# Performance work log

Measured on AMD Instinct MI355X. Metric: run time of the kernel, lower is better.

The kernel has to match this reference:

```python
import jax, jax.numpy as jnp
import numpy as np

N = 30000      # num nodes
E = 600000     # num edges
D = 128        # feature dim (all layers)
R = 7          # num_relation
G = 16         # num graphs in batch
L = 3          # num layers (hidden_dims = [128,128,128])


def setup_inputs() -> dict:
    key = jax.random.key(0)
    ks = jax.random.split(key, 10)
    x = jax.random.normal(ks[0], (N, D), dtype=jnp.float32)
    node_in = jax.random.randint(ks[1], (E,), 0, N)
    node_out = jax.random.randint(ks[2], (E,), 0, N)
    relation = jax.random.randint(ks[3], (E,), 0, R)
    edge_weight = jax.random.uniform(ks[4], (E,), dtype=jnp.float32)
    node2graph = jnp.sort(jax.random.randint(ks[5], (N,), 0, G))
    # learned params: per-layer relational linear (R*D -> D) and self-loop linear (D -> D)
    Wr = jax.random.normal(ks[6], (L, R * D, D), dtype=jnp.float32) * 0.02
    br = jnp.zeros((L, D), dtype=jnp.float32)
    Wl = jax.random.normal(ks[7], (L, D, D), dtype=jnp.float32) * 0.02
    bl = jnp.zeros((L, D), dtype=jnp.float32)
    return dict(x=x, node_in=node_in, node_out=node_out, relation=relation,
                edge_weight=edge_weight, node2graph=node2graph,
                Wr=Wr, br=br, Wl=Wl, bl=bl)


def reference(x, node_in, node_out, relation, edge_weight, node2graph, Wr, br, Wl, bl):
    # relation-indexed destination segment: node_out * R + relation
    seg = node_out * R + relation            # (E,)
    ew = edge_weight[:, None]                # (E, 1)
    h = x
    for i in range(L):
        msg = h[node_in] * ew                                         # gather + weight, (E, D)
        upd = jax.ops.segment_sum(msg, seg, num_segments=N * R)       # scatter_add, (N*R, D)
        upd = upd.reshape(N, R * D)                                   # per-relation concat
        h = jax.nn.relu(upd @ Wr[i] + br[i] + h @ Wl[i] + bl[i])      # linear + self-loop + act
    node_feature = h                                                  # (N, D)
    graph_feature = jax.ops.segment_sum(node_feature, node2graph, num_segments=G)  # sum readout
    return graph_feature, node_feature
```

## Files before the change

### kernel.cpp

```cpp
#include <hip/hip_runtime.h>
#include <hip/hip_bf16.h>

#define NN 30000
#define NE 600000
#define DD 128
#define RR 7
#define GG 16
#define LL 3

#define NB64 ((NN + 63) / 64)

typedef short bf16x8 __attribute__((ext_vector_type(8)));
typedef float f32x4  __attribute__((ext_vector_type(4)));

__device__ __forceinline__ unsigned short f2bf(float f) {
    unsigned u = __float_as_uint(f);
    unsigned r = (u + 0x7fffu + ((u >> 16) & 1u)) >> 16;
    return (unsigned short)r;
}
__device__ __forceinline__ float bf2f(unsigned short b) {
    return __uint_as_float(((unsigned)b) << 16);
}
__device__ __forceinline__ ushort2 pk2bf(float a, float b) {
    __hip_bfloat162 t = __float22bfloat162_rn(make_float2(a, b));
    return *(ushort2*)&t;
}

__device__ __forceinline__ void gl_lds16(const void* g, void* l) {
    __builtin_amdgcn_global_load_lds(
        (const __attribute__((address_space(1))) void*)g,
        (__attribute__((address_space(3))) void*)l, 16, 0, 0);
}

__global__ __launch_bounds__(256) void pack_weights(
    const float* __restrict__ Wl,
    const float* __restrict__ Wr,
    unsigned short* __restrict__ Bw)
{
    int t = blockIdx.x * 256 + threadIdx.x;
    if (t >= LL * 1024 * DD) return;
    int l = t >> 17;
    int rem = t & 131071;
    int n = rem >> 7;
    int k = rem & 127;
    float v;
    if (n < DD) {
        v = Wl[(size_t)l * DD * DD + k * DD + n];
    } else {
        int q = n - DD;
        v = Wr[(size_t)l * RR * DD * DD + (size_t)((q >> 7) * DD + k) * DD + (q & 127)];
    }
    Bw[(size_t)l * 1024 * DD + n * DD + k] = f2bf(v);
}

__global__ __launch_bounds__(256) void convert_bf16(
    const float* __restrict__ in, unsigned short* __restrict__ out, int n4)
{
    int i = blockIdx.x * 256 + threadIdx.x;
    if (i >= n4) return;
    float4 v = ((const float4*)in)[i];
    ushort2 lo = pk2bf(v.x, v.y);
    ushort2 hi = pk2bf(v.z, v.w);
    ((ushort4*)out)[i] = make_ushort4(lo.x, lo.y, hi.x, hi.y);
}

#define ASTR 128
__global__ __launch_bounds__(256) void gemm_mfma(
    const unsigned short* __restrict__ hb,
    const unsigned short* __restrict__ Bw,
    const float* __restrict__ br,
    const float* __restrict__ bl,
    unsigned short* __restrict__ haccb,
    unsigned short* __restrict__ Zb,
    int N)
{
    __shared__ unsigned short As[64 * ASTR];
    __shared__ unsigned short Bs[128 * ASTR];

    const int tid  = threadIdx.x;
    const int wave = tid >> 6;
    const int lane = tid & 63;
    const int quad = lane >> 4;
    const int l16  = lane & 15;
    const int row0 = blockIdx.x * 64;
    const int col0 = blockIdx.y * 128;

#pragma unroll
    for (int i = 0; i < 4; ++i) {
        int g = i * 4 + wave;
        gl_lds16(hb + (size_t)(row0 + g * 4) * DD + lane * 8,
                 As + g * 512);
    }
#pragma unroll
    for (int i = 0; i < 8; ++i) {
        int g = i * 4 + wave;
        gl_lds16(Bw + (size_t)col0 * DD + (size_t)g * 512 + lane * 8,
                 Bs + g * 512);
    }
    __syncthreads();

    f32x4 acc[4][2];
#pragma unroll
    for (int mt = 0; mt < 4; ++mt)
#pragma unroll
        for (int nt = 0; nt < 2; ++nt)
            acc[mt][nt] = (f32x4){0.f, 0.f, 0.f, 0.f};

    const unsigned short* As_l = As + l16 * ASTR;
    const unsigned short* Bs_l = Bs + (wave * 32 + l16) * ASTR;

#pragma unroll
    for (int kc = 0; kc < 4; ++kc) {
        int ko = kc * 32 + quad * 8;
        bf16x8 a0 = *(const bf16x8*)(As_l + 0 * 16 * ASTR + ko);
        bf16x8 a1 = *(const bf16x8*)(As_l + 1 * 16 * ASTR + ko);
        bf16x8 a2 = *(const bf16x8*)(As_l + 2 * 16 * ASTR + ko);
        bf16x8 a3 = *(const bf16x8*)(As_l + 3 * 16 * ASTR + ko);
        bf16x8 b0 = *(const bf16x8*)(Bs_l + 0 * 16 * ASTR + ko);
        bf16x8 b1 = *(const bf16x8*)(Bs_l + 1 * 16 * ASTR + ko);
        acc[0][0] = __builtin_amdgcn_mfma_f32_16x16x32_bf16(a0, b0, acc[0][0], 0, 0, 0);
        acc[1][0] = __builtin_amdgcn_mfma_f32_16x16x32_bf16(a1, b0, acc[1][0], 0, 0, 0);
        acc[2][0] = __builtin_amdgcn_mfma_f32_16x16x32_bf16(a2, b0, acc[2][0], 0, 0, 0);
        acc[3][0] = __builtin_amdgcn_mfma_f32_16x16x32_bf16(a3, b0, acc[3][0], 0, 0, 0);
        acc[0][1] = __builtin_amdgcn_mfma_f32_16x16x32_bf16(a0, b1, acc[0][1], 0, 0, 0);
        acc[1][1] = __builtin_amdgcn_mfma_f32_16x16x32_bf16(a1, b1, acc[1][1], 0, 0, 0);
        acc[2][1] = __builtin_amdgcn_mfma_f32_16x16x32_bf16(a2, b1, acc[2][1], 0, 0, 0);
        acc[3][1] = __builtin_amdgcn_mfma_f32_16x16x32_bf16(a3, b1, acc[3][1], 0, 0, 0);
    }

    const int ncol = wave * 32 + l16;
    if (col0 == 0) {
        float bias0 = br[ncol] + bl[ncol];
        float bias1 = br[ncol + 16] + bl[ncol + 16];
#pragma unroll
        for (int mt = 0; mt < 4; ++mt) {
#pragma unroll
            for (int reg = 0; reg < 4; ++reg) {
                int row = row0 + mt * 16 + quad * 4 + reg;
                if (row < N) {
                    ushort2 p = pk2bf(acc[mt][0][reg] + bias0,
                                      acc[mt][1][reg] + bias1);
                    haccb[(size_t)row * DD + ncol]      = p.x;
                    haccb[(size_t)row * DD + ncol + 16] = p.y;
                }
            }
        }
    } else {
        const int zc = col0 - DD + ncol;
#pragma unroll
        for (int mt = 0; mt < 4; ++mt) {
#pragma unroll
            for (int reg = 0; reg < 4; ++reg) {
                int row = row0 + mt * 16 + quad * 4 + reg;
                if (row < N) {
                    ushort2 p = pk2bf(acc[mt][0][reg], acc[mt][1][reg]);
                    Zb[(size_t)row * (RR * DD) + zc]      = p.x;
                    Zb[(size_t)row * (RR * DD) + zc + 16] = p.y;
                }
            }
        }
    }
}

__global__ __launch_bounds__(256) void bucket_hist(
    const int* __restrict__ node_out, int* __restrict__ bcnt, int E)
{
    int e = blockIdx.x * 256 + threadIdx.x;
    if (e < E) atomicAdd(&bcnt[(node_out[e] >> 6) * 16], 1);
}

__global__ __launch_bounds__(512) void bucket_scan(
    const int* __restrict__ bcnt, int* __restrict__ bstart,
    int* __restrict__ bcur, int nb)
{
    __shared__ int s[512];
    int t = threadIdx.x;
    int v = (t < nb) ? bcnt[t * 16] : 0;
    s[t] = v;
    __syncthreads();
#pragma unroll
    for (int off = 1; off < 512; off <<= 1) {
        int u = (t >= off) ? s[t - off] : 0;
        __syncthreads();
        s[t] += u;
        __syncthreads();
    }
    if (t <= nb) {
        int excl = s[t] - v;
        bstart[t] = excl;
        if (t < nb) bcur[t * 16] = excl;
    }
}

__global__ __launch_bounds__(256) void bucket_scatter(
    const int* __restrict__ node_in,
    const int* __restrict__ node_out,
    const int* __restrict__ relation,
    const float* __restrict__ ew,
    int* __restrict__ bcur,
    int2* __restrict__ tmp,
    int E)
{
    int e = blockIdx.x * 256 + threadIdx.x;
    if (e >= E) return;
    int o = node_out[e];
    int pos = atomicAdd(&bcur[(o >> 6) * 16], 1);
    tmp[pos] = make_int2(((o & 63) << 18) | (node_in[e] << 3) | relation[e],
                         __float_as_int(ew[e]));
}

__global__ __launch_bounds__(256) void bucket_sort(
    const int2* __restrict__ tmp,
    const int* __restrict__ bstart,
    int2* __restrict__ meta,
    int* __restrict__ start,
    int N)
{
    __shared__ int hist[64];
    __shared__ int scan[64];
    __shared__ int cur[64];
    const int b = blockIdx.x;
    const int t = threadIdx.x;
    const int s0 = bstart[b];
    const int s1 = bstart[b + 1];

    if (t < 64) hist[t] = 0;
    __syncthreads();
    for (int i = s0 + t; i < s1; i += 256)
        atomicAdd(&hist[((unsigned)tmp[i].x) >> 18], 1);
    __syncthreads();

    int v = (t < 64) ? hist[t] : 0;
    if (t < 64) scan[t] = v;
    __syncthreads();
#pragma unroll
    for (int off = 1; off < 64; off <<= 1) {
        int u = (t < 64 && t >= off) ? scan[t - off] : 0;
        __syncthreads();
        if (t < 64) scan[t] += u;
        __syncthreads();
    }
    if (t < 64) {
        int excl = scan[t] - v;
        cur[t] = s0 + excl;
        int node = b * 64 + t;
        if (node <= N) start[node] = s0 + excl;
    }
    __syncthreads();

    for (int i = s0 + t; i < s1; i += 256) {
        int2 m = tmp[i];
        int j = ((unsigned)m.x) >> 18;
        int pos = atomicAdd(&cur[j], 1);
        int key = m.x & 0x3ffff;
        int in = key >> 3, rel = key & 7;
        meta[pos] = make_int2((in * RR + rel) << 7, m.y);
    }
}

__global__ __launch_bounds__(256) void aggregate(
    const unsigned short* __restrict__ Zb,
    const int* __restrict__ start,
    const int2* __restrict__ meta,
    const unsigned short* __restrict__ haccb,
    float* __restrict__ out_f32,
    unsigned short* __restrict__ out_bf16,
    int N)
{
    int wid = (blockIdx.x * 256 + threadIdx.x) >> 6;
    int lane = threadIdx.x & 63;
    if (wid >= N) return;

    int e0 = start[wid];
    int e1 = start[wid + 1];

    float accx = 0.f, accy = 0.f;
    int e = e0;
    for (; e + 8 <= e1; e += 8) {
        unsigned u[8]; float wt[8];
#pragma unroll
        for (int j = 0; j < 8; ++j) {
            int2 m = meta[e + j];
            u[j] = *(const unsigned*)(Zb + m.x + lane * 2);
            wt[j] = __int_as_float(m.y);
        }
#pragma unroll
        for (int j = 0; j < 8; ++j) {
            accx = fmaf(wt[j], __uint_as_float(u[j] << 16), accx);
            accy = fmaf(wt[j], __uint_as_float(u[j] & 0xffff0000u), accy);
        }
    }
    for (; e + 2 <= e1; e += 2) {
        int2 m0 = meta[e];
        int2 m1 = meta[e + 1];
        unsigned u0 = *(const unsigned*)(Zb + m0.x + lane * 2);
        unsigned u1 = *(const unsigned*)(Zb + m1.x + lane * 2);
        float w0 = __int_as_float(m0.y), w1 = __int_as_float(m1.y);
        accx = fmaf(w0, __uint_as_float(u0 << 16), accx);
        accy = fmaf(w0, __uint_as_float(u0 & 0xffff0000u), accy);
        accx = fmaf(w1, __uint_as_float(u1 << 16), accx);
        accy = fmaf(w1, __uint_as_float(u1 & 0xffff0000u), accy);
    }
    if (e < e1) {
        int2 m = meta[e];
        unsigned u = *(const unsigned*)(Zb + m.x + lane * 2);
        float wt = __int_as_float(m.y);
        accx = fmaf(wt, __uint_as_float(u << 16), accx);
        accy = fmaf(wt, __uint_as_float(u & 0xffff0000u), accy);
    }

    unsigned bu = *(const unsigned*)(haccb + (size_t)wid * DD + lane * 2);
    float ox = fmaxf(bf2f((unsigned short)(bu & 0xffffu)) + accx, 0.f);
    float oy = fmaxf(bf2f((unsigned short)(bu >> 16)) + accy, 0.f);
    if (out_f32) {
        *(float2*)(out_f32 + (size_t)wid * DD + lane * 2) = make_float2(ox, oy);
    }
    if (out_bf16) {
        ushort2 o = pk2bf(ox, oy);
        *(ushort2*)(out_bf16 + (size_t)wid * DD + lane * 2) = o;
    }
}

__global__ __launch_bounds__(256) void graph_sum(
    const float* __restrict__ nf,
    const int* __restrict__ n2g,
    float* __restrict__ gf,
    int N)
{
    int t = blockIdx.x * 256 + threadIdx.x;
    int chunk = t >> 5;
    int lane = t & 31;
    int n0 = chunk * 16;
    if (n0 >= N) return;
    int nend = n0 + 16; if (nend > N) nend = N;

    float4 acc = make_float4(0.f, 0.f, 0.f, 0.f);
    int curg = n2g[n0];
    for (int n = n0; n < nend; ++n) {
        int g = n2g[n];
        if (g != curg) {
            float* dst = gf + (size_t)curg * DD + lane * 4;
            atomicAdd(dst + 0, acc.x); atomicAdd(dst + 1, acc.y);
            atomicAdd(dst + 2, acc.z); atomicAdd(dst + 3, acc.w);
            acc = make_float4(0.f, 0.f, 0.f, 0.f);
            curg = g;
        }
        float4 v = *(const float4*)(nf + (size_t)n * DD + lane * 4);
        acc.x += v.x; acc.y += v.y; acc.z += v.z; acc.w += v.w;
    }
    float* dst = gf + (size_t)curg * DD + lane * 4;
    atomicAdd(dst + 0, acc.x); atomicAdd(dst + 1, acc.y);
    atomicAdd(dst + 2, acc.z); atomicAdd(dst + 3, acc.w);
}

extern "C" void kernel_launch(void* const* d_in, const int* in_sizes, int n_in,
                              void* d_out, int out_size, void* d_ws, size_t ws_size,
                              hipStream_t stream)
{
    const float* x        = (const float*)d_in[0];
    const int*   node_in  = (const int*)d_in[1];
    const int*   node_out = (const int*)d_in[2];
    const int*   relation = (const int*)d_in[3];
    const float* ew       = (const float*)d_in[4];
    const int*   n2g      = (const int*)d_in[5];
    const float* Wr       = (const float*)d_in[6];
    const float* br       = (const float*)d_in[7];
    const float* Wl       = (const float*)d_in[8];
    const float* bl       = (const float*)d_in[9];

    float* out = (float*)d_out;
    float* gf = out;
    float* nf = out + GG * DD;

    char* w = (char*)d_ws;
    unsigned short* Zb   = (unsigned short*)w; w += (size_t)NN * RR * DD * 2;
    unsigned short* haccb= (unsigned short*)w; w += (size_t)NN * DD * 2;
    unsigned short* hbA  = (unsigned short*)w; w += (size_t)NN * DD * 2;
    unsigned short* hbB  = (unsigned short*)w; w += (size_t)NN * DD * 2;
    unsigned short* Bw   = (unsigned short*)w; w += (size_t)LL * 1024 * DD * 2;
    int2*  meta   = (int2*)w;                  w += (size_t)NE * 8;
    int2*  tmp    = (int2*)w;                  w += (size_t)NE * 8;
    int*   start  = (int*)w;                   w += (size_t)(NN + 1) * 4 + 60;
    int*   bcnt   = (int*)w;                   w += (size_t)NB64 * 16 * 4 + 64;
    int*   bcur   = (int*)w;                   w += (size_t)NB64 * 16 * 4 + 64;
    int*   bstart = (int*)w;                   w += (size_t)(NB64 + 1) * 4 + 60;

    const int N = NN, E = NE;

    pack_weights<<<(LL * 1024 * DD + 255) / 256, 256, 0, stream>>>(Wl, Wr, Bw);
    convert_bf16<<<(N * DD / 4 + 255) / 256, 256, 0, stream>>>(x, hbA, N * DD / 4);

    hipMemsetAsync(bcnt, 0, (size_t)NB64 * 16 * sizeof(int), stream);
    bucket_hist<<<(E + 255) / 256, 256, 0, stream>>>(node_out, bcnt, E);
    bucket_scan<<<1, 512, 0, stream>>>(bcnt, bstart, bcur, NB64);
    bucket_scatter<<<(E + 255) / 256, 256, 0, stream>>>(
        node_in, node_out, relation, ew, bcur, tmp, E);
    bucket_sort<<<NB64, 256, 0, stream>>>(tmp, bstart, meta, start, N);

    dim3 ggrid((N + 63) / 64, 8);
    unsigned short* hin = hbA;
    unsigned short* hnext = hbB;
    for (int l = 0; l < LL; ++l) {
        const float* br_l = br + (size_t)l * DD;
        const float* bl_l = bl + (size_t)l * DD;
        const unsigned short* Bw_l = Bw + (size_t)l * 1024 * DD;

        gemm_mfma<<<ggrid, 256, 0, stream>>>(hin, Bw_l, br_l, bl_l, haccb, Zb, N);

        bool last = (l == LL - 1);
        aggregate<<<(N * 64 + 255) / 256, 256, 0, stream>>>(
            Zb, start, meta, haccb,
            last ? nf : (float*)nullptr,
            last ? (unsigned short*)nullptr : hnext, N);

        unsigned short* t = hin; hin = hnext; hnext = t;
    }

    hipMemsetAsync(gf, 0, (size_t)GG * DD * sizeof(float), stream);
    int chunks = (N + 15) / 16;
    graph_sum<<<(chunks * 32 + 255) / 256, 256, 0, stream>>>(nf, n2g, gf, N);
}
```

Measured before the change: 344.4 us.

## Aggregate raw features per relation before transforming with one fused GEMM

Swaps the order of the two steps. Each layer used to run the per-relation linear transform first and then gather the wide transformed rows for every edge. Now each node first gathers and sums the narrow bf16 input rows per (node, relation) into a message buffer, and a single GEMM with K=1024 then applies the relational and self-loop weights together, with bias and ReLU fused in. Per-edge gathers now hit a small feature table instead of the large transformed one. The bucket sort now orders edges by node and relation with per-relation start offsets, and the memsets are folded into existing kernels. The trade-offs are that the GEMM grid becomes 469 blocks doing an unpipelined K loop, and each wave's gather loop is split into seven short per-relation chains.

```diff
diff --git a/kernel.cpp b/kernel.cpp
--- a/kernel.cpp
+++ b/kernel.cpp
@@ -9,6 +9,8 @@
 #define LL 3
 
 #define NB64 ((NN + 63) / 64)
+#define NROW (NB64 * 64)
+#define MS   (RR * DD)
 
 typedef short bf16x8 __attribute__((ext_vector_type(8)));
 typedef float f32x4  __attribute__((ext_vector_type(4)));
@@ -18,9 +20,6 @@
     unsigned r = (u + 0x7fffu + ((u >> 16) & 1u)) >> 16;
     return (unsigned short)r;
 }
-__device__ __forceinline__ float bf2f(unsigned short b) {
-    return __uint_as_float(((unsigned)b) << 16);
-}
 __device__ __forceinline__ ushort2 pk2bf(float a, float b) {
     __hip_bfloat162 t = __float22bfloat162_rn(make_float2(a, b));
     return *(ushort2*)&t;
@@ -35,131 +34,37 @@
 __global__ __launch_bounds__(256) void pack_weights(
     const float* __restrict__ Wl,
     const float* __restrict__ Wr,
-    unsigned short* __restrict__ Bw)
+    unsigned short* __restrict__ Bw2,
+    int* __restrict__ bcnt)
 {
     int t = blockIdx.x * 256 + threadIdx.x;
-    if (t >= LL * 1024 * DD) return;
-    int l = t >> 17;
-    int rem = t & 131071;
-    int n = rem >> 7;
-    int k = rem & 127;
+    if (t < NB64 * 16) bcnt[t] = 0;
+    if (t >= LL * 8 * DD * DD) return;
+    int kp = t & 127;
+    int n  = (t >> 7) & 127;
+    int kc = (t >> 14) & 7;
+    int l  = t >> 17;
+    int k  = kc * 128 + kp;
     float v;
-    if (n < DD) {
-        v = Wl[(size_t)l * DD * DD + k * DD + n];
-    } else {
-        int q = n - DD;
-        v = Wr[(size_t)l * RR * DD * DD + (size_t)((q >> 7) * DD + k) * DD + (q & 127)];
-    }
-    Bw[(size_t)l * 1024 * DD + n * DD + k] = f2bf(v);
+    if (k < MS) v = Wr[(size_t)l * MS * DD + (size_t)k * DD + n];
+    else        v = Wl[(size_t)l * DD * DD + (size_t)(k - MS) * DD + n];
+    Bw2[(size_t)l * 8 * DD * DD + (size_t)kc * DD * DD + n * DD + kp] = f2bf(v);
 }
 
 __global__ __launch_bounds__(256) void convert_bf16(
-    const float* __restrict__ in, unsigned short* __restrict__ out, int n4)
+    const float* __restrict__ in, unsigned short* __restrict__ out,
+    float* __restrict__ gf, int n4)
 {
     int i = blockIdx.x * 256 + threadIdx.x;
+    if (blockIdx.x == 0) {
+#pragma unroll
+        for (int j = 0; j < 8; ++j) gf[threadIdx.x + j * 256] = 0.f;
+    }
     if (i >= n4) return;
     float4 v = ((const float4*)in)[i];
     ushort2 lo = pk2bf(v.x, v.y);
     ushort2 hi = pk2bf(v.z, v.w);
     ((ushort4*)out)[i] = make_ushort4(lo.x, lo.y, hi.x, hi.y);
-}
-
-#define ASTR 128
-__global__ __launch_bounds__(256) void gemm_mfma(
-    const unsigned short* __restrict__ hb,
-    const unsigned short* __restrict__ Bw,
-    const float* __restrict__ br,
-    const float* __restrict__ bl,
-    unsigned short* __restrict__ haccb,
-    unsigned short* __restrict__ Zb,
-    int N)
-{
-    __shared__ unsigned short As[64 * ASTR];
-    __shared__ unsigned short Bs[128 * ASTR];
-
-    const int tid  = threadIdx.x;
-    const int wave = tid >> 6;
-    const int lane = tid & 63;
-    const int quad = lane >> 4;
-    const int l16  = lane & 15;
-    const int row0 = blockIdx.x * 64;
-    const int col0 = blockIdx.y * 128;
-
-#pragma unroll
-    for (int i = 0; i < 4; ++i) {
-        int g = i * 4 + wave;
-        gl_lds16(hb + (size_t)(row0 + g * 4) * DD + lane * 8,
-                 As + g * 512);
-    }
-#pragma unroll
-    for (int i = 0; i < 8; ++i) {
-        int g = i * 4 + wave;
-        gl_lds16(Bw + (size_t)col0 * DD + (size_t)g * 512 + lane * 8,
-                 Bs + g * 512);
-    }
-    __syncthreads();
-
-    f32x4 acc[4][2];
-#pragma unroll
-    for (int mt = 0; mt < 4; ++mt)
-#pragma unroll
-        for (int nt = 0; nt < 2; ++nt)
-            acc[mt][nt] = (f32x4){0.f, 0.f, 0.f, 0.f};
-
-    const unsigned short* As_l = As + l16 * ASTR;
-    const unsigned short* Bs_l = Bs + (wave * 32 + l16) * ASTR;
-
-#pragma unroll
-    for (int kc = 0; kc < 4; ++kc) {
-        int ko = kc * 32 + quad * 8;
-        bf16x8 a0 = *(const bf16x8*)(As_l + 0 * 16 * ASTR + ko);
-        bf16x8 a1 = *(const bf16x8*)(As_l + 1 * 16 * ASTR + ko);
-        bf16x8 a2 = *(const bf16x8*)(As_l + 2 * 16 * ASTR + ko);
-        bf16x8 a3 = *(const bf16x8*)(As_l + 3 * 16 * ASTR + ko);
-        bf16x8 b0 = *(const bf16x8*)(Bs_l + 0 * 16 * ASTR + ko);
-        bf16x8 b1 = *(const bf16x8*)(Bs_l + 1 * 16 * ASTR + ko);
-        acc[0][0] = __builtin_amdgcn_mfma_f32_16x16x32_bf16(a0, b0, acc[0][0], 0, 0, 0);
-        acc[1][0] = __builtin_amdgcn_mfma_f32_16x16x32_bf16(a1, b0, acc[1][0], 0, 0, 0);
-        acc[2][0] = __builtin_amdgcn_mfma_f32_16x16x32_bf16(a2, b0, acc[2][0], 0, 0, 0);
-        acc[3][0] = __builtin_amdgcn_mfma_f32_16x16x32_bf16(a3, b0, acc[3][0], 0, 0, 0);
-        acc[0][1] = __builtin_amdgcn_mfma_f32_16x16x32_bf16(a0, b1, acc[0][1], 0, 0, 0);
-        acc[1][1] = __builtin_amdgcn_mfma_f32_16x16x32_bf16(a1, b1, acc[1][1], 0, 0, 0);
-        acc[2][1] = __builtin_amdgcn_mfma_f32_16x16x32_bf16(a2, b1, acc[2][1], 0, 0, 0);
-        acc[3][1] = __builtin_amdgcn_mfma_f32_16x16x32_bf16(a3, b1, acc[3][1], 0, 0, 0);
-    }
-
-    const int ncol = wave * 32 + l16;
-    if (col0 == 0) {
-        float bias0 = br[ncol] + bl[ncol];
-        float bias1 = br[ncol + 16] + bl[ncol + 16];
-#pragma unroll
-        for (int mt = 0; mt < 4; ++mt) {
-#pragma unroll
-            for (int reg = 0; reg < 4; ++reg) {
-                int row = row0 + mt * 16 + quad * 4 + reg;
-                if (row < N) {
-                    ushort2 p = pk2bf(acc[mt][0][reg] + bias0,
-                                      acc[mt][1][reg] + bias1);
-                    haccb[(size_t)row * DD + ncol]      = p.x;
-                    haccb[(size_t)row * DD + ncol + 16] = p.y;
-                }
-            }
-        }
-    } else {
-        const int zc = col0 - DD + ncol;
-#pragma unroll
-        for (int mt = 0; mt < 4; ++mt) {
-#pragma unroll
-            for (int reg = 0; reg < 4; ++reg) {
-                int row = row0 + mt * 16 + quad * 4 + reg;
-                if (row < N) {
-                    ushort2 p = pk2bf(acc[mt][0][reg], acc[mt][1][reg]);
-                    Zb[(size_t)row * (RR * DD) + zc]      = p.x;
-                    Zb[(size_t)row * (RR * DD) + zc + 16] = p.y;
-                }
-            }
-        }
-    }
 }
 
 __global__ __launch_bounds__(256) void bucket_hist(
@@ -205,7 +110,7 @@
     if (e >= E) return;
     int o = node_out[e];
     int pos = atomicAdd(&bcur[(o >> 6) * 16], 1);
-    tmp[pos] = make_int2(((o & 63) << 18) | (node_in[e] << 3) | relation[e],
+    tmp[pos] = make_int2(((o & 63) << 21) | (relation[e] << 18) | node_in[e],
                          __float_as_int(ew[e]));
 }
 
@@ -213,111 +118,205 @@
     const int2* __restrict__ tmp,
     const int* __restrict__ bstart,
     int2* __restrict__ meta,
-    int* __restrict__ start,
+    int* __restrict__ start2,
     int N)
 {
-    __shared__ int hist[64];
-    __shared__ int scan[64];
-    __shared__ int cur[64];
+    __shared__ int hist[512];
+    __shared__ int excl[512];
+    __shared__ int cur[512];
+    __shared__ int ssum[256];
     const int b = blockIdx.x;
     const int t = threadIdx.x;
     const int s0 = bstart[b];
     const int s1 = bstart[b + 1];
 
-    if (t < 64) hist[t] = 0;
+    hist[t] = 0; hist[t + 256] = 0;
     __syncthreads();
     for (int i = s0 + t; i < s1; i += 256)
         atomicAdd(&hist[((unsigned)tmp[i].x) >> 18], 1);
     __syncthreads();
 
-    int v = (t < 64) ? hist[t] : 0;
-    if (t < 64) scan[t] = v;
-    __syncthreads();
-#pragma unroll
-    for (int off = 1; off < 64; off <<= 1) {
-        int u = (t < 64 && t >= off) ? scan[t - off] : 0;
-        __syncthreads();
-        if (t < 64) scan[t] += u;
-        __syncthreads();
-    }
-    if (t < 64) {
-        int excl = scan[t] - v;
-        cur[t] = s0 + excl;
-        int node = b * 64 + t;
-        if (node <= N) start[node] = s0 + excl;
+    int a0 = hist[2 * t], a1 = hist[2 * t + 1];
+    ssum[t] = a0 + a1;
+    __syncthreads();
+#pragma unroll
+    for (int off = 1; off < 256; off <<= 1) {
+        int u = (t >= off) ? ssum[t - off] : 0;
+        __syncthreads();
+        ssum[t] += u;
+        __syncthreads();
+    }
+    int base = (t == 0) ? 0 : ssum[t - 1];
+    excl[2 * t] = base;
+    excl[2 * t + 1] = base + a0;
+    cur[2 * t] = s0 + base;
+    cur[2 * t + 1] = s0 + base + a0;
+    __syncthreads();
+
+    {
+        int node0 = b * 64 + (t >> 3) * 2;
+        int k0 = 2 * t, k1 = 2 * t + 1;
+        int n0 = b * 64 + (k0 >> 3), n1 = b * 64 + (k1 >> 3);
+        if (n0 < N) start2[n0 * 8 + (k0 & 7)] = s0 + excl[k0];
+        if (n1 < N) start2[n1 * 8 + (k1 & 7)] = s0 + excl[k1];
+        (void)node0;
     }
     __syncthreads();
 
     for (int i = s0 + t; i < s1; i += 256) {
         int2 m = tmp[i];
-        int j = ((unsigned)m.x) >> 18;
-        int pos = atomicAdd(&cur[j], 1);
-        int key = m.x & 0x3ffff;
-        int in = key >> 3, rel = key & 7;
-        meta[pos] = make_int2((in * RR + rel) << 7, m.y);
-    }
-}
-
-__global__ __launch_bounds__(256) void aggregate(
-    const unsigned short* __restrict__ Zb,
-    const int* __restrict__ start,
+        int key = ((unsigned)m.x) >> 18;
+        int pos = atomicAdd(&cur[key], 1);
+        int src = m.x & 0x3ffff;
+        meta[pos] = make_int2(src << 7, m.y);
+    }
+}
+
+__global__ __launch_bounds__(256) void aggregate_msg(
+    const unsigned short* __restrict__ hb,
+    const int* __restrict__ start2,
     const int2* __restrict__ meta,
-    const unsigned short* __restrict__ haccb,
-    float* __restrict__ out_f32,
-    unsigned short* __restrict__ out_bf16,
+    unsigned short* __restrict__ msg,
     int N)
 {
     int wid = (blockIdx.x * 256 + threadIdx.x) >> 6;
     int lane = threadIdx.x & 63;
     if (wid >= N) return;
 
-    int e0 = start[wid];
-    int e1 = start[wid + 1];
-
-    float accx = 0.f, accy = 0.f;
-    int e = e0;
-    for (; e + 8 <= e1; e += 8) {
-        unsigned u[8]; float wt[8];
-#pragma unroll
-        for (int j = 0; j < 8; ++j) {
-            int2 m = meta[e + j];
-            u[j] = *(const unsigned*)(Zb + m.x + lane * 2);
-            wt[j] = __int_as_float(m.y);
-        }
-#pragma unroll
-        for (int j = 0; j < 8; ++j) {
-            accx = fmaf(wt[j], __uint_as_float(u[j] << 16), accx);
-            accy = fmaf(wt[j], __uint_as_float(u[j] & 0xffff0000u), accy);
-        }
-    }
-    for (; e + 2 <= e1; e += 2) {
-        int2 m0 = meta[e];
-        int2 m1 = meta[e + 1];
-        unsigned u0 = *(const unsigned*)(Zb + m0.x + lane * 2);
-        unsigned u1 = *(const unsigned*)(Zb + m1.x + lane * 2);
-        float w0 = __int_as_float(m0.y), w1 = __int_as_float(m1.y);
-        accx = fmaf(w0, __uint_as_float(u0 << 16), accx);
-        accy = fmaf(w0, __uint_as_float(u0 & 0xffff0000u), accy);
-        accx = fmaf(w1, __uint_as_float(u1 << 16), accx);
-        accy = fmaf(w1, __uint_as_float(u1 & 0xffff0000u), accy);
-    }
-    if (e < e1) {
-        int2 m = meta[e];
-        unsigned u = *(const unsigned*)(Zb + m.x + lane * 2);
-        float wt = __int_as_float(m.y);
-        accx = fmaf(wt, __uint_as_float(u << 16), accx);
-        accy = fmaf(wt, __uint_as_float(u & 0xffff0000u), accy);
-    }
-
-    unsigned bu = *(const unsigned*)(haccb + (size_t)wid * DD + lane * 2);
-    float ox = fmaxf(bf2f((unsigned short)(bu & 0xffffu)) + accx, 0.f);
-    float oy = fmaxf(bf2f((unsigned short)(bu >> 16)) + accy, 0.f);
-    if (out_f32) {
-        *(float2*)(out_f32 + (size_t)wid * DD + lane * 2) = make_float2(ox, oy);
-    }
-    if (out_bf16) {
-        ushort2 o = pk2bf(ox, oy);
-        *(ushort2*)(out_bf16 + (size_t)wid * DD + lane * 2) = o;
+    unsigned short* mrow = msg + (size_t)wid * MS + lane * 2;
+#pragma unroll
+    for (int r = 0; r < RR; ++r) {
+        int e0 = start2[wid * 8 + r];
+        int e1 = start2[wid * 8 + r + 1];
+        float ax = 0.f, ay = 0.f;
+        int e = e0;
+        for (; e + 4 <= e1; e += 4) {
+            int2 m0 = meta[e + 0];
+            int2 m1 = meta[e + 1];
+            int2 m2 = meta[e + 2];
+            int2 m3 = meta[e + 3];
+            unsigned u0 = *(const unsigned*)(hb + m0.x + lane * 2);
+            unsigned u1 = *(const unsigned*)(hb + m1.x + lane * 2);
+            unsigned u2 = *(const unsigned*)(hb + m2.x + lane * 2);
+            unsigned u3 = *(const unsigned*)(hb + m3.x + lane * 2);
+            float w0 = __int_as_float(m0.y), w1 = __int_as_float(m1.y);
+            float w2 = __int_as_float(m2.y), w3 = __int_as_float(m3.y);
+            ax = fmaf(w0, __uint_as_float(u0 << 16), ax);
+            ay = fmaf(w0, __uint_as_float(u0 & 0xffff0000u), ay);
+            ax = fmaf(w1, __uint_as_float(u1 << 16), ax);
+            ay = fmaf(w1, __uint_as_float(u1 & 0xffff0000u), ay);
+            ax = fmaf(w2, __uint_as_float(u2 << 16), ax);
+            ay = fmaf(w2, __uint_as_float(u2 & 0xffff0000u), ay);
+            ax = fmaf(w3, __uint_as_float(u3 << 16), ax);
+            ay = fmaf(w3, __uint_as_float(u3 & 0xffff0000u), ay);
+        }
+        for (; e < e1; ++e) {
+            int2 m = meta[e];
+            unsigned u = *(const unsigned*)(hb + m.x + lane * 2);
+            float wt = __int_as_float(m.y);
+            ax = fmaf(wt, __uint_as_float(u << 16), ax);
+            ay = fmaf(wt, __uint_as_float(u & 0xffff0000u), ay);
+        }
+        *(ushort2*)(mrow + r * DD) = pk2bf(ax, ay);
+    }
+}
+
+__global__ __launch_bounds__(256) void gemm2(
+    const unsigned short* __restrict__ msg,
+    const unsigned short* __restrict__ hb,
+    const unsigned short* __restrict__ Bw2l,
+    const float* __restrict__ br,
+    const float* __restrict__ bl,
+    unsigned short* __restrict__ out_bf16,
+    float* __restrict__ out_f32,
+    int N)
+{
+    __shared__ unsigned short As[64 * 128];
+    __shared__ unsigned short Bs[128 * 128];
+
+    const int tid  = threadIdx.x;
+    const int wave = tid >> 6;
+    const int lane = tid & 63;
+    const int quad = lane >> 4;
+    const int l16  = lane & 15;
+    const int row0 = blockIdx.x * 64;
+
+    f32x4 acc[4][2];
+#pragma unroll
+    for (int mt = 0; mt < 4; ++mt)
+#pragma unroll
+        for (int nt = 0; nt < 2; ++nt)
+            acc[mt][nt] = (f32x4){0.f, 0.f, 0.f, 0.f};
+
+    const int arow = lane >> 4;
+    const int acol = (lane & 15) * 8;
+
+#pragma unroll
+    for (int kc = 0; kc < 8; ++kc) {
+        const unsigned short* asrc;
+        int astr;
+        if (kc < 7) { asrc = msg + (size_t)row0 * MS + kc * 128; astr = MS; }
+        else        { asrc = hb  + (size_t)row0 * DD;            astr = DD; }
+#pragma unroll
+        for (int i = 0; i < 4; ++i) {
+            int g = i * 4 + wave;
+            gl_lds16(asrc + (size_t)(g * 4 + arow) * astr + acol,
+                     As + g * 512);
+        }
+        const unsigned short* bsrc = Bw2l + (size_t)kc * DD * DD;
+#pragma unroll
+        for (int i = 0; i < 8; ++i) {
+            int g = i * 4 + wave;
+            gl_lds16(bsrc + (size_t)g * 512 + lane * 8,
+                     Bs + g * 512);
+        }
+        __syncthreads();
+
+        const unsigned short* As_l = As + l16 * 128;
+        const unsigned short* Bs_l = Bs + (wave * 32 + l16) * 128;
+#pragma unroll
+        for (int kci = 0; kci < 4; ++kci) {
+            int ko = kci * 32 + quad * 8;
+            bf16x8 a0 = *(const bf16x8*)(As_l + 0 * 16 * 128 + ko);
+            bf16x8 a1 = *(const bf16x8*)(As_l + 1 * 16 * 128 + ko);
+            bf16x8 a2 = *(const bf16x8*)(As_l + 2 * 16 * 128 + ko);
+            bf16x8 a3 = *(const bf16x8*)(As_l + 3 * 16 * 128 + ko);
+            bf16x8 b0 = *(const bf16x8*)(Bs_l + 0 * 16 * 128 + ko);
+            bf16x8 b1 = *(const bf16x8*)(Bs_l + 1 * 16 * 128 + ko);
+            acc[0][0] = __builtin_amdgcn_mfma_f32_16x16x32_bf16(a0, b0, acc[0][0], 0, 0, 0);
+            acc[1][0] = __builtin_amdgcn_mfma_f32_16x16x32_bf16(a1, b0, acc[1][0], 0, 0, 0);
+            acc[2][0] = __builtin_amdgcn_mfma_f32_16x16x32_bf16(a2, b0, acc[2][0], 0, 0, 0);
+            acc[3][0] = __builtin_amdgcn_mfma_f32_16x16x32_bf16(a3, b0, acc[3][0], 0, 0, 0);
+            acc[0][1] = __builtin_amdgcn_mfma_f32_16x16x32_bf16(a0, b1, acc[0][1], 0, 0, 0);
+            acc[1][1] = __builtin_amdgcn_mfma_f32_16x16x32_bf16(a1, b1, acc[1][1], 0, 0, 0);
+            acc[2][1] = __builtin_amdgcn_mfma_f32_16x16x32_bf16(a2, b1, acc[2][1], 0, 0, 0);
+            acc[3][1] = __builtin_amdgcn_mfma_f32_16x16x32_bf16(a3, b1, acc[3][1], 0, 0, 0);
+        }
+        __syncthreads();
+    }
+
+    const int ncol = wave * 32 + l16;
+    float bias0 = br[ncol] + bl[ncol];
+    float bias1 = br[ncol + 16] + bl[ncol + 16];
+#pragma unroll
+    for (int mt = 0; mt < 4; ++mt) {
+#pragma unroll
+        for (int reg = 0; reg < 4; ++reg) {
+            int row = row0 + mt * 16 + quad * 4 + reg;
+            if (row < N) {
+                float v0 = fmaxf(acc[mt][0][reg] + bias0, 0.f);
+                float v1 = fmaxf(acc[mt][1][reg] + bias1, 0.f);
+                if (out_bf16) {
+                    ushort2 p = pk2bf(v0, v1);
+                    out_bf16[(size_t)row * DD + ncol]      = p.x;
+                    out_bf16[(size_t)row * DD + ncol + 16] = p.y;
+                }
+                if (out_f32) {
+                    out_f32[(size_t)row * DD + ncol]      = v0;
+                    out_f32[(size_t)row * DD + ncol + 16] = v1;
+                }
+            }
+        }
     }
 }
 
@@ -373,50 +372,47 @@
     float* nf = out + GG * DD;
 
     char* w = (char*)d_ws;
-    unsigned short* Zb   = (unsigned short*)w; w += (size_t)NN * RR * DD * 2;
-    unsigned short* haccb= (unsigned short*)w; w += (size_t)NN * DD * 2;
-    unsigned short* hbA  = (unsigned short*)w; w += (size_t)NN * DD * 2;
-    unsigned short* hbB  = (unsigned short*)w; w += (size_t)NN * DD * 2;
-    unsigned short* Bw   = (unsigned short*)w; w += (size_t)LL * 1024 * DD * 2;
+    unsigned short* msg  = (unsigned short*)w; w += (size_t)NROW * MS * 2;
+    unsigned short* hbA  = (unsigned short*)w; w += (size_t)NROW * DD * 2;
+    unsigned short* hbB  = (unsigned short*)w; w += (size_t)NROW * DD * 2;
+    unsigned short* Bw2  = (unsigned short*)w; w += (size_t)LL * 8 * DD * DD * 2;
     int2*  meta   = (int2*)w;                  w += (size_t)NE * 8;
     int2*  tmp    = (int2*)w;                  w += (size_t)NE * 8;
-    int*   start  = (int*)w;                   w += (size_t)(NN + 1) * 4 + 60;
+    int*   start2 = (int*)w;                   w += (size_t)NROW * 8 * 4;
     int*   bcnt   = (int*)w;                   w += (size_t)NB64 * 16 * 4 + 64;
     int*   bcur   = (int*)w;                   w += (size_t)NB64 * 16 * 4 + 64;
     int*   bstart = (int*)w;                   w += (size_t)(NB64 + 1) * 4 + 60;
 
     const int N = NN, E = NE;
 
-    pack_weights<<<(LL * 1024 * DD + 255) / 256, 256, 0, stream>>>(Wl, Wr, Bw);
-    convert_bf16<<<(N * DD / 4 + 255) / 256, 256, 0, stream>>>(x, hbA, N * DD / 4);
-
-    hipMemsetAsync(bcnt, 0, (size_t)NB64 * 16 * sizeof(int), stream);
+    pack_weights<<<(LL * 8 * DD * DD + 255) / 256, 256, 0, stream>>>(Wl, Wr, Bw2, bcnt);
+    convert_bf16<<<(N * DD / 4 + 255) / 256, 256, 0, stream>>>(x, hbA, gf, N * DD / 4);
+
     bucket_hist<<<(E + 255) / 256, 256, 0, stream>>>(node_out, bcnt, E);
     bucket_scan<<<1, 512, 0, stream>>>(bcnt, bstart, bcur, NB64);
     bucket_scatter<<<(E + 255) / 256, 256, 0, stream>>>(
         node_in, node_out, relation, ew, bcur, tmp, E);
-    bucket_sort<<<NB64, 256, 0, stream>>>(tmp, bstart, meta, start, N);
-
-    dim3 ggrid((N + 63) / 64, 8);
+    bucket_sort<<<NB64, 256, 0, stream>>>(tmp, bstart, meta, start2, N);
+
     unsigned short* hin = hbA;
     unsigned short* hnext = hbB;
     for (int l = 0; l < LL; ++l) {
         const float* br_l = br + (size_t)l * DD;
         const float* bl_l = bl + (size_t)l * DD;
-        const unsigned short* Bw_l = Bw + (size_t)l * 1024 * DD;
-
-        gemm_mfma<<<ggrid, 256, 0, stream>>>(hin, Bw_l, br_l, bl_l, haccb, Zb, N);
+        const unsigned short* Bw2_l = Bw2 + (size_t)l * 8 * DD * DD;
+
+        aggregate_msg<<<(N * 64 + 255) / 256, 256, 0, stream>>>(
+            hin, start2, meta, msg, N);
 
         bool last = (l == LL - 1);
-        aggregate<<<(N * 64 + 255) / 256, 256, 0, stream>>>(
-            Zb, start, meta, haccb,
-            last ? nf : (float*)nullptr,
-            last ? (unsigned short*)nullptr : hnext, N);
+        gemm2<<<NB64, 256, 0, stream>>>(
+            msg, hin, Bw2_l, br_l, bl_l,
+            last ? (unsigned short*)nullptr : hnext,
+            last ? nf : (float*)nullptr, N);
 
         unsigned short* t = hin; hin = hnext; hnext = t;
     }
 
-    hipMemsetAsync(gf, 0, (size_t)GG * DD * sizeof(float), stream);
     int chunks = (N + 15) / 16;
     graph_sum<<<(chunks * 32 + 255) / 256, 256, 0, stream>>>(nf, n2g, gf, N);
 }
```

Result: slower. 414.0 us (+20.2%).
